# Kernel optimization log

Hardware: AMD Instinct MI355X
Metric: run time of the kernel (lower is better)

The kernel has to match this reference:

```python
import jax, jax.numpy as jnp
import numpy as np
from jax import lax

EPS = 1e-5  # nn.BatchNorm2d default eps


def _binarize_act(x):
    # out = sign(x).detach() - clip(x).detach() + clip(x)  (STE)
    c = jnp.clip(x, -1.0, 1.0)
    return c + lax.stop_gradient(jnp.sign(x) - c)


def _binarize_weight(w):
    # w.data = w.fp.sign().add(0.01).sign()  -> {-1,+1}, zeros map to +1.
    # Autograd in torch sees identity wrt the parameter (data swap), i.e. STE.
    wb = jnp.sign(jnp.sign(w) + 0.01)
    return w + lax.stop_gradient(wb - w)


def setup_inputs() -> dict:
    key = jax.random.key(0)
    k1, k2, k3, k4 = jax.random.split(key, 4)
    N, Cin, Cout, H, W = 16, 32, 32, 256, 256
    return {
        "x": jax.random.normal(k1, (N, Cin, H, W), dtype=jnp.float32),
        "weight": jax.random.normal(k2, (Cout, Cin, 3, 3), dtype=jnp.float32),
        "gamma": jnp.ones((Cout,), dtype=jnp.float32),
        "beta": jnp.zeros((Cout,), dtype=jnp.float32),
        "running_mean": jax.random.normal(k3, (Cout,), dtype=jnp.float32) * 0.1,
        "running_var": jax.random.uniform(k4, (Cout,), dtype=jnp.float32) + 0.5,
    }


def reference(x, weight, gamma, beta, running_mean, running_var):
    xb = _binarize_act(x)
    wb = _binarize_weight(weight)
    # 3x3, stride 1, padding 1 -> SAME spatial size
    out = lax.conv_general_dilated(
        xb, wb,
        window_strides=(1, 1),
        padding=((1, 1), (1, 1)),
        dimension_numbers=("NCHW", "OIHW", "NCHW"),
    )
    # BatchNorm2d (inference form with running stats), then ReLU
    inv = gamma / jnp.sqrt(running_var + EPS)  # [C]
    out = out * inv[None, :, None, None] + (beta - running_mean * inv)[None, :, None, None]
    return jax.nn.relu(out)
```

## Files before the change

### kernel.cpp

```cpp
#include <hip/hip_runtime.h>
#include <stdint.h>

#define NB   16
#define CIN  32
#define COUT 32
#define HH   256
#define WW   256
#define HWSZ (HH * WW)
#define EPSV 1e-5f

__global__ void pack_w_kernel(const float* __restrict__ wt,
                              uint32_t* __restrict__ pw) {
    const int j = threadIdx.x;
    if (j < COUT * 9) {
        const int o = j / 9, t = j % 9;
        uint32_t bits = 0;
#pragma unroll
        for (int c = 0; c < CIN; ++c) {
            const float v = wt[(o * CIN + c) * 9 + t];
            bits |= (v < 0.f) ? (1u << c) : 0u;
        }
        pw[j] = bits;
    }
}

__global__ __launch_bounds__(256) void biconv_fused(
    const float* __restrict__ x, const uint32_t* __restrict__ pw,
    const float* __restrict__ gamma, const float* __restrict__ beta,
    const float* __restrict__ rmean, const float* __restrict__ rvar,
    float* __restrict__ out) {
    const uint32_t bid = blockIdx.x;
    const uint32_t wg  = ((bid & 7u) << 9) | (bid >> 3);
    const int n = wg >> 8;
    const int h = wg & 255;
    const int tid = threadIdx.x;

    __shared__ uint4    wsh4[COUT * 3];
    __shared__ float    sc[COUT], bi[COUT];
    __shared__ uint32_t tile[3][WW + 2];

    if (tid < 192) {
        const int r  = tid >> 6;
        const int q  = tid & 63;
        const int hr = h + r - 1;
        uint32_t b0 = 0, b1 = 0, b2 = 0, b3 = 0;
        if (hr >= 0 && hr < HH) {
            const float* xp = x + (size_t)n * (CIN * HWSZ) + hr * WW + (q << 2);
#pragma unroll
            for (int c = 0; c < CIN; ++c) {
                const float4 v = *reinterpret_cast<const float4*>(xp + c * HWSZ);
                b0 |= (v.x < 0.f) ? (1u << c) : 0u;
                b1 |= (v.y < 0.f) ? (1u << c) : 0u;
                b2 |= (v.z < 0.f) ? (1u << c) : 0u;
                b3 |= (v.w < 0.f) ? (1u << c) : 0u;
            }
        }
        const int wbase = (q << 2) + 1;
        tile[r][wbase + 0] = b0;
        tile[r][wbase + 1] = b1;
        tile[r][wbase + 2] = b2;
        tile[r][wbase + 3] = b3;
    } else {
        const int t2 = tid - 192;
        uint32_t* wshw = reinterpret_cast<uint32_t*>(wsh4);
#pragma unroll
        for (int k = 0; k < 6; ++k) {
            const int i = t2 + 64 * k;
            const int o = i / 12, t = i % 12;
            wshw[i] = (t < 9) ? pw[o * 9 + t] : 0u;
        }
        if (t2 < COUT) {
            const float inv = gamma[t2] * rsqrtf(rvar[t2] + EPSV);
            sc[t2] = inv;
            bi[t2] = beta[t2] - rmean[t2] * inv;
        }
        if (t2 >= 32 && t2 < 35) {
            const int r = t2 - 32;
            tile[r][0] = 0u;
            tile[r][WW + 1] = 0u;
        }
    }
    __syncthreads();

    const int w = tid;
    uint32_t p[9], m[9];
    const bool rv[3] = { h > 0, true, h < HH - 1 };
    const bool cv[3] = { w > 0, true, w < WW - 1 };
    int nv = 0;
#pragma unroll
    for (int dh = 0; dh < 3; ++dh) {
#pragma unroll
        for (int dw = 0; dw < 3; ++dw) {
            const int t = dh * 3 + dw;
            p[t] = tile[dh][w + dw];
            const bool v = rv[dh] && cv[dw];
            m[t] = v ? 0xffffffffu : 0u;
            nv += v ? 1 : 0;
        }
    }
    const float base = (float)(nv * 32);

    float* outp = out + (size_t)n * (COUT * HWSZ) + h * WW + w;
#pragma unroll
    for (int o = 0; o < COUT; ++o) {
        const uint4 wa = wsh4[o * 3 + 0];
        const uint4 wb = wsh4[o * 3 + 1];
        const uint4 wc = wsh4[o * 3 + 2];
        int acc = 0;
        acc += __popc((p[0] ^ wa.x) & m[0]);
        acc += __popc((p[1] ^ wa.y) & m[1]);
        acc += __popc((p[2] ^ wa.z) & m[2]);
        acc += __popc((p[3] ^ wa.w) & m[3]);
        acc += __popc((p[4] ^ wb.x) & m[4]);
        acc += __popc((p[5] ^ wb.y) & m[5]);
        acc += __popc((p[6] ^ wb.z) & m[6]);
        acc += __popc((p[7] ^ wb.w) & m[7]);
        acc += __popc((p[8] ^ wc.x) & m[8]);
        const float s = base - 2.0f * (float)acc;
        const float r = fmaf(s, sc[o], bi[o]);
        __builtin_nontemporal_store(r > 0.f ? r : 0.f, outp + o * HWSZ);
    }
}

extern "C" void kernel_launch(void* const* d_in, const int* in_sizes, int n_in,
                              void* d_out, int out_size, void* d_ws, size_t ws_size,
                              hipStream_t stream) {
    const float* x     = (const float*)d_in[0];
    const float* wt    = (const float*)d_in[1];
    const float* gamma = (const float*)d_in[2];
    const float* beta  = (const float*)d_in[3];
    const float* rmean = (const float*)d_in[4];
    const float* rvar  = (const float*)d_in[5];
    float* out = (float*)d_out;

    uint32_t* pw = (uint32_t*)d_ws;

    pack_w_kernel<<<dim3(1), dim3(288), 0, stream>>>(wt, pw);
    biconv_fused<<<dim3(NB * HH), dim3(256), 0, stream>>>(x, pw, gamma, beta,
                                                          rmean, rvar, out);
}
```

Measured before the change: 53.62 us.

## Compute four output rows per block and precompute padding offsets

Each workgroup now binarizes a six-row halo tile and produces four output rows, cutting redundant input reads and setup per row. Boundary masks are removed by having padded taps read zero bits and correcting with a per-class offset table computed in the weight-packing kernel. Sign extraction uses the integer sign bit. The grid shrinks fourfold, which may reduce latency hiding.

```diff
diff --git a/kernel.cpp b/kernel.cpp
--- a/kernel.cpp
+++ b/kernel.cpp
@@ -8,9 +8,14 @@
 #define WW   256
 #define HWSZ (HH * WW)
 #define EPSV 1e-5f
+#define RR   4
+#define SR   (RR + 2)
+#define TSTRIDE 260
 
-__global__ void pack_w_kernel(const float* __restrict__ wt,
-                              uint32_t* __restrict__ pw) {
+__global__ __launch_bounds__(288) void pack_w_kernel(const float* __restrict__ wt,
+                                                     uint32_t* __restrict__ pw,
+                                                     float* __restrict__ offf) {
+    __shared__ uint32_t pws[COUT * 9];
     const int j = threadIdx.x;
     if (j < COUT * 9) {
         const int o = j / 9, t = j % 9;
@@ -21,104 +26,129 @@
             bits |= (v < 0.f) ? (1u << c) : 0u;
         }
         pw[j] = bits;
+        pws[j] = bits;
+    }
+    __syncthreads();
+    {
+        const int cls = j / COUT;
+        const int o   = j % COUT;
+        const int rc = cls / 3, cc = cls % 3;
+        int inv = 0, nv = 0;
+#pragma unroll
+        for (int dh = 0; dh < 3; ++dh)
+#pragma unroll
+            for (int dw = 0; dw < 3; ++dw) {
+                const bool bad = (rc == 0 && dh == 0) || (rc == 2 && dh == 2) ||
+                                 (cc == 0 && dw == 0) || (cc == 2 && dw == 2);
+                if (bad) inv += __popc(pws[o * 9 + dh * 3 + dw]);
+                else     nv++;
+            }
+        offf[j] = (float)(nv * 32 + 2 * inv);
     }
 }
 
 __global__ __launch_bounds__(256) void biconv_fused(
-    const float* __restrict__ x, const uint32_t* __restrict__ pw,
+    const uint32_t* __restrict__ x, const uint32_t* __restrict__ pw,
+    const float* __restrict__ offf,
     const float* __restrict__ gamma, const float* __restrict__ beta,
     const float* __restrict__ rmean, const float* __restrict__ rvar,
     float* __restrict__ out) {
     const uint32_t bid = blockIdx.x;
-    const uint32_t wg  = ((bid & 7u) << 9) | (bid >> 3);
-    const int n = wg >> 8;
-    const int h = wg & 255;
+    const uint32_t wg  = ((bid & 7u) << 7) | (bid >> 3);
+    const int n   = wg >> 6;
+    const int hb  = wg & 63;
+    const int h0  = hb << 2;
     const int tid = threadIdx.x;
 
     __shared__ uint4    wsh4[COUT * 3];
+    __shared__ float    offsh[9 * COUT];
     __shared__ float    sc[COUT], bi[COUT];
-    __shared__ uint32_t tile[3][WW + 2];
+    __shared__ uint32_t tile[SR][TSTRIDE];
 
-    if (tid < 192) {
-        const int r  = tid >> 6;
-        const int q  = tid & 63;
-        const int hr = h + r - 1;
-        uint32_t b0 = 0, b1 = 0, b2 = 0, b3 = 0;
-        if (hr >= 0 && hr < HH) {
-            const float* xp = x + (size_t)n * (CIN * HWSZ) + hr * WW + (q << 2);
+    uint32_t* wshw = reinterpret_cast<uint32_t*>(wsh4);
 #pragma unroll
-            for (int c = 0; c < CIN; ++c) {
-                const float4 v = *reinterpret_cast<const float4*>(xp + c * HWSZ);
-                b0 |= (v.x < 0.f) ? (1u << c) : 0u;
-                b1 |= (v.y < 0.f) ? (1u << c) : 0u;
-                b2 |= (v.z < 0.f) ? (1u << c) : 0u;
-                b3 |= (v.w < 0.f) ? (1u << c) : 0u;
+    for (int i = tid; i < COUT * 12; i += 256) {
+        const int o = i / 12, t = i % 12;
+        wshw[i] = (t < 9) ? pw[o * 9 + t] : 0u;
+    }
+#pragma unroll
+    for (int i = tid; i < 9 * COUT; i += 256) offsh[i] = offf[i];
+    if (tid < COUT) {
+        const float inv = gamma[tid] * rsqrtf(rvar[tid] + EPSV);
+        sc[tid] = inv;
+        bi[tid] = beta[tid] - rmean[tid] * inv;
+    }
+    if (tid < SR) {
+        tile[tid][WW + 0] = 0u; tile[tid][WW + 1] = 0u;
+        tile[tid][WW + 2] = 0u; tile[tid][WW + 3] = 0u;
+    }
+
+    const uint32_t* xn = x + (size_t)n * (CIN * HWSZ);
+#pragma unroll
+    for (int it = 0; it < 2; ++it) {
+        const int q = tid + it * 256;
+        if (q < SR * 64) {
+            const int r  = q >> 6;
+            const int qq = q & 63;
+            const int hr = h0 - 1 + r;
+            uint32_t b0 = 0, b1 = 0, b2 = 0, b3 = 0;
+            if (hr >= 0 && hr < HH) {
+                const uint32_t* xp = xn + hr * WW + (qq << 2);
+#pragma unroll
+                for (int c = 0; c < CIN; ++c) {
+                    const uint4 v = *reinterpret_cast<const uint4*>(xp + (size_t)c * HWSZ);
+                    b0 |= (v.x >> 31) << c;
+                    b1 |= (v.y >> 31) << c;
+                    b2 |= (v.z >> 31) << c;
+                    b3 |= (v.w >> 31) << c;
+                }
             }
-        }
-        const int wbase = (q << 2) + 1;
-        tile[r][wbase + 0] = b0;
-        tile[r][wbase + 1] = b1;
-        tile[r][wbase + 2] = b2;
-        tile[r][wbase + 3] = b3;
-    } else {
-        const int t2 = tid - 192;
-        uint32_t* wshw = reinterpret_cast<uint32_t*>(wsh4);
-#pragma unroll
-        for (int k = 0; k < 6; ++k) {
-            const int i = t2 + 64 * k;
-            const int o = i / 12, t = i % 12;
-            wshw[i] = (t < 9) ? pw[o * 9 + t] : 0u;
-        }
-        if (t2 < COUT) {
-            const float inv = gamma[t2] * rsqrtf(rvar[t2] + EPSV);
-            sc[t2] = inv;
-            bi[t2] = beta[t2] - rmean[t2] * inv;
-        }
-        if (t2 >= 32 && t2 < 35) {
-            const int r = t2 - 32;
-            tile[r][0] = 0u;
-            tile[r][WW + 1] = 0u;
+            *reinterpret_cast<uint4*>(&tile[r][qq << 2]) = make_uint4(b0, b1, b2, b3);
         }
     }
     __syncthreads();
 
-    const int w = tid;
-    uint32_t p[9], m[9];
-    const bool rv[3] = { h > 0, true, h < HH - 1 };
-    const bool cv[3] = { w > 0, true, w < WW - 1 };
-    int nv = 0;
+    const int w  = tid;
+    const int wl = (w == 0) ? WW : (w - 1);
+    uint32_t p[SR][3];
 #pragma unroll
-    for (int dh = 0; dh < 3; ++dh) {
+    for (int j = 0; j < SR; ++j) {
+        p[j][0] = tile[j][wl];
+        p[j][1] = tile[j][w];
+        p[j][2] = tile[j][w + 1];
+    }
+    const int ccls = (w == 0) ? 0 : ((w == WW - 1) ? 2 : 1);
+    int offidx[RR];
 #pragma unroll
-        for (int dw = 0; dw < 3; ++dw) {
-            const int t = dh * 3 + dw;
-            p[t] = tile[dh][w + dw];
-            const bool v = rv[dh] && cv[dw];
-            m[t] = v ? 0xffffffffu : 0u;
-            nv += v ? 1 : 0;
-        }
+    for (int r = 0; r < RR; ++r) {
+        const int h  = h0 + r;
+        const int rc = (h == 0) ? 0 : ((h == HH - 1) ? 2 : 1);
+        offidx[r] = (rc * 3 + ccls) * COUT;
     }
-    const float base = (float)(nv * 32);
-
-    float* outp = out + (size_t)n * (COUT * HWSZ) + h * WW + w;
-#pragma unroll
+    float* outp = out + (size_t)n * (COUT * HWSZ) + (size_t)h0 * WW + w;
+#pragma unroll 4
     for (int o = 0; o < COUT; ++o) {
         const uint4 wa = wsh4[o * 3 + 0];
         const uint4 wb = wsh4[o * 3 + 1];
         const uint4 wc = wsh4[o * 3 + 2];
-        int acc = 0;
-        acc += __popc((p[0] ^ wa.x) & m[0]);
-        acc += __popc((p[1] ^ wa.y) & m[1]);
-        acc += __popc((p[2] ^ wa.z) & m[2]);
-        acc += __popc((p[3] ^ wa.w) & m[3]);
-        acc += __popc((p[4] ^ wb.x) & m[4]);
-        acc += __popc((p[5] ^ wb.y) & m[5]);
-        acc += __popc((p[6] ^ wb.z) & m[6]);
-        acc += __popc((p[7] ^ wb.w) & m[7]);
-        acc += __popc((p[8] ^ wc.x) & m[8]);
-        const float s = base - 2.0f * (float)acc;
-        const float r = fmaf(s, sc[o], bi[o]);
-        __builtin_nontemporal_store(r > 0.f ? r : 0.f, outp + o * HWSZ);
+        const float scv = sc[o], biv = bi[o];
+#pragma unroll
+        for (int r = 0; r < RR; ++r) {
+            int acc;
+            acc  = __popc(p[r + 0][0] ^ wa.x);
+            acc += __popc(p[r + 0][1] ^ wa.y);
+            acc += __popc(p[r + 0][2] ^ wa.z);
+            acc += __popc(p[r + 1][0] ^ wa.w);
+            acc += __popc(p[r + 1][1] ^ wb.x);
+            acc += __popc(p[r + 1][2] ^ wb.y);
+            acc += __popc(p[r + 2][0] ^ wb.z);
+            acc += __popc(p[r + 2][1] ^ wb.w);
+            acc += __popc(p[r + 2][2] ^ wc.x);
+            const float s = fmaf(-2.0f, (float)acc, offsh[offidx[r] + o]);
+            const float v = fmaf(s, scv, biv);
+            __builtin_nontemporal_store(v > 0.f ? v : 0.f,
+                                        outp + (size_t)o * HWSZ + r * WW);
+        }
     }
 }
 
@@ -133,9 +163,10 @@
     const float* rvar  = (const float*)d_in[5];
     float* out = (float*)d_out;
 
-    uint32_t* pw = (uint32_t*)d_ws;
+    uint32_t* pw   = (uint32_t*)d_ws;
+    float*    offf = (float*)(pw + 288);
 
-    pack_w_kernel<<<dim3(1), dim3(288), 0, stream>>>(wt, pw);
-    biconv_fused<<<dim3(NB * HH), dim3(256), 0, stream>>>(x, pw, gamma, beta,
-                                                          rmean, rvar, out);
+    pack_w_kernel<<<dim3(1), dim3(288), 0, stream>>>(wt, pw, offf);
+    biconv_fused<<<dim3(NB * HH / RR), dim3(256), 0, stream>>>(
+        (const uint32_t*)x, pw, offf, gamma, beta, rmean, rvar, out);
 }
```

New measurement: 63.49 us. +18.4%, slower.
